# Kernel optimization log

Measured on AMD Instinct MI355X. Metric: run time of the kernel, lower is better.

The kernel has to match this reference:

```python
import jax, jax.numpy as jnp
import numpy as np

LN_EPS = 1e-5
GATE_EPS = 1e-9
TOP_K = 2
CAP_FACTOR = 1.0


def reference(x, gamma, beta, wg, W1, b1, W2, b2):
    B, S, H = x.shape
    E = wg.shape[1]
    T = B * S
    K = TOP_K
    C = int(np.ceil(K * T / E * CAP_FACTOR))  # per-expert capacity

    xf = x.reshape(T, H)
    # LayerNorm
    mu = jnp.mean(xf, axis=-1, keepdims=True)
    var = jnp.mean(jnp.square(xf - mu), axis=-1, keepdims=True)
    xn = (xf - mu) * jax.lax.rsqrt(var + LN_EPS) * gamma + beta

    # Gating (DeepSpeed top-k gate, softmax over experts)
    logits = xn @ wg                       # [T,E]
    gates = jax.nn.softmax(logits, axis=-1)
    vals, idx = jax.lax.top_k(gates, K)    # [T,K]

    # Capacity-aware positions: slot j priorities come after slots <j counts
    counts = jnp.zeros((E,), jnp.int32)
    pos_l, keep_l = [], []
    for j in range(K):
        oh = jax.nn.one_hot(idx[:, j], E, dtype=jnp.int32)  # [T,E]
        loc = jnp.cumsum(oh, axis=0) - 1 + counts[None, :]
        pos = jnp.sum(loc * oh, axis=1)                      # [T]
        counts = counts + jnp.sum(oh, axis=0)
        pos_l.append(pos)
        keep_l.append(pos < C)
    pos_k = jnp.stack(pos_l, axis=1)                         # [T,K]
    keep_k = jnp.stack(keep_l, axis=1)                       # [T,K]

    # Normalize kept gate values (DeepSpeed normalizes after capacity drop)
    kept = vals * keep_k.astype(vals.dtype)
    w = kept / (jnp.sum(kept, axis=1, keepdims=True) + GATE_EPS)  # [T,K]

    # Load-balancing aux loss (top-1 assignment counts, DeepSpeed style)
    me = jnp.mean(gates, axis=0)
    ce = jnp.mean(jax.nn.one_hot(idx[:, 0], E, dtype=gates.dtype), axis=0)
    l_aux = jnp.mean(me * ce) * E * E

    # Dispatch: scatter tokens into [E, C+1, H]; dropped tokens go to slot C (discarded)
    buf = jnp.zeros((E, C + 1, H), xn.dtype)
    pos_pad = jnp.where(keep_k, pos_k, C)                    # [T,K]
    for j in range(K):
        buf = buf.at[idx[:, j], pos_pad[:, j]].add(xn)

    # Grouped expert MLP
    h1 = jax.nn.gelu(jnp.einsum('ech,ehf->ecf', buf, W1) + b1[:, None, :], approximate=False)
    y = jnp.einsum('ecf,efh->ech', h1, W2) + b2[:, None, :]   # [E,C+1,H]

    # Combine: gather each token's expert outputs, weight, sum
    outf = jnp.zeros((T, H), x.dtype)
    for j in range(K):
        outf = outf + w[:, j, None] * y[idx[:, j], pos_pad[:, j]]

    out = x + outf.reshape(B, S, H)
    return out, l_aux, counts.astype(jnp.float32)


def setup_inputs() -> dict:
    key = jax.random.key(0)
    ks = jax.random.split(key, 6)
    H, E, F = 1024, 8, 4096
    x = jax.random.normal(ks[0], (2, 2048, H), jnp.float32)
    return {
        'x': x,
        'gamma': jnp.ones((H,), jnp.float32),
        'beta': jnp.zeros((H,), jnp.float32),
        'wg': jax.random.normal(ks[1], (H, E), jnp.float32) * 0.02,
        'W1': jax.random.normal(ks[2], (E, H, F), jnp.float32) * 0.02,
        'b1': jnp.zeros((E, F), jnp.float32),
        'W2': jax.random.normal(ks[3], (E, F, H), jnp.float32) * 0.02,
        'b2': jnp.zeros((E, H), jnp.float32),
    }
```

## Files before the change

### kernel.cpp

```cpp
#include <hip/hip_runtime.h>
#include <hip/hip_bf16.h>
#include <math.h>


#define T_TOK 4096
#define HD 1024
#define NE 8
#define FD 4096
#define CAPN 1024

typedef __attribute__((ext_vector_type(8))) short short8;
typedef __attribute__((ext_vector_type(4))) float f32x4;

__device__ __forceinline__ unsigned short f2b(float f) {
  __hip_bfloat16 h = __float2bfloat16(f);
  unsigned short u;
  __builtin_memcpy(&u, &h, 2);
  return u;
}

__global__ __launch_bounds__(256) void k_ln_gate(
    const float* __restrict__ x, const float* __restrict__ gamma,
    const float* __restrict__ beta, const float* __restrict__ wg,
    unsigned short* __restrict__ xn, float* __restrict__ gates,
    float2* __restrict__ vals, int2* __restrict__ eidx) {
  const int t = blockIdx.x;
  const int tid = threadIdx.x;
  const int lane = tid & 63, wid = tid >> 6;
  __shared__ float red[4];
  __shared__ float pr[4][8];

  const float4 v = ((const float4*)(x + (size_t)t * HD))[tid];
  float s = v.x + v.y + v.z + v.w;
#pragma unroll
  for (int o = 32; o > 0; o >>= 1) s += __shfl_down(s, o);
  if (lane == 0) red[wid] = s;
  __syncthreads();
  const float mean = (red[0] + red[1] + red[2] + red[3]) * (1.0f / HD);
  float dv[4];
  dv[0] = v.x - mean; dv[1] = v.y - mean; dv[2] = v.z - mean; dv[3] = v.w - mean;
  float q = dv[0]*dv[0] + dv[1]*dv[1] + dv[2]*dv[2] + dv[3]*dv[3];
  __syncthreads();
#pragma unroll
  for (int o = 32; o > 0; o >>= 1) q += __shfl_down(q, o);
  if (lane == 0) red[wid] = q;
  __syncthreads();
  const float var = (red[0] + red[1] + red[2] + red[3]) * (1.0f / HD);
  const float rs = 1.0f / sqrtf(var + 1e-5f);

  const float4 gm = ((const float4*)gamma)[tid];
  const float4 bt = ((const float4*)beta)[tid];
  float xv[4];
  xv[0] = dv[0] * rs * gm.x + bt.x;
  xv[1] = dv[1] * rs * gm.y + bt.y;
  xv[2] = dv[2] * rs * gm.z + bt.z;
  xv[3] = dv[3] * rs * gm.w + bt.w;
  ushort4 o4;
  o4.x = f2b(xv[0]); o4.y = f2b(xv[1]); o4.z = f2b(xv[2]); o4.w = f2b(xv[3]);
  ((ushort4*)(xn + (size_t)t * HD))[tid] = o4;

  float p[8];
#pragma unroll
  for (int e = 0; e < 8; e++) p[e] = 0.f;
  const int c0 = tid * 4;
#pragma unroll
  for (int i = 0; i < 4; i++) {
    const float4 w0 = ((const float4*)(wg + (size_t)(c0 + i) * NE))[0];
    const float4 w1 = ((const float4*)(wg + (size_t)(c0 + i) * NE))[1];
    p[0] += xv[i] * w0.x; p[1] += xv[i] * w0.y;
    p[2] += xv[i] * w0.z; p[3] += xv[i] * w0.w;
    p[4] += xv[i] * w1.x; p[5] += xv[i] * w1.y;
    p[6] += xv[i] * w1.z; p[7] += xv[i] * w1.w;
  }
#pragma unroll
  for (int e = 0; e < 8; e++)
#pragma unroll
    for (int o = 32; o > 0; o >>= 1) p[e] += __shfl_down(p[e], o);
  if (lane == 0) {
#pragma unroll
    for (int e = 0; e < 8; e++) pr[wid][e] = p[e];
  }
  __syncthreads();
  if (tid == 0) {
    float lg[8];
#pragma unroll
    for (int e = 0; e < 8; e++) lg[e] = pr[0][e] + pr[1][e] + pr[2][e] + pr[3][e];
    float mx = lg[0];
#pragma unroll
    for (int e = 1; e < 8; e++) mx = fmaxf(mx, lg[e]);
    float ex[8], sum = 0.f;
#pragma unroll
    for (int e = 0; e < 8; e++) { ex[e] = expf(lg[e] - mx); sum += ex[e]; }
    const float inv = 1.0f / sum;
    float g[8];
#pragma unroll
    for (int e = 0; e < 8; e++) { g[e] = ex[e] * inv; gates[(size_t)t * 8 + e] = g[e]; }
    int i0 = 0;
    for (int e = 1; e < 8; e++) if (g[e] > g[i0]) i0 = e;
    int i1 = (i0 == 0) ? 1 : 0;
    for (int e = 0; e < 8; e++) if (e != i0 && g[e] > g[i1]) i1 = e;
    vals[t] = make_float2(g[i0], g[i1]);
    eidx[t] = make_int2(i0, i1);
  }
}

__global__ __launch_bounds__(512) void k_scan(
    const int2* __restrict__ eidx, const float* __restrict__ gates,
    int* __restrict__ ppad, float* __restrict__ out_tail) {
  __shared__ short se0[T_TOK], se1[T_TOK];
  __shared__ int cc[2][64][8];
  __shared__ int cb[2][64][8];
  __shared__ float gsum[8][8];
  __shared__ int ctot[8], c0tot[8];
  const int tid = threadIdx.x, lane = tid & 63, wid = tid >> 6;
  for (int i = tid; i < T_TOK; i += 512) {
    int2 e2 = eidx[i];
    se0[i] = (short)e2.x; se1[i] = (short)e2.y;
  }
  __syncthreads();
  for (int c = wid * 8; c < wid * 8 + 8; ++c) {
    const int t = c * 64 + lane;
    const int e0 = se0[t], e1 = se1[t];
#pragma unroll
    for (int e = 0; e < 8; ++e) {
      unsigned long long m0 = __ballot(e0 == e);
      unsigned long long m1 = __ballot(e1 == e);
      if (lane == e) { cc[0][c][e] = __popcll(m0); cc[1][c][e] = __popcll(m1); }
    }
  }
  __syncthreads();
  {
    const int e = wid;
    int v0 = cc[0][lane][e], v1 = cc[1][lane][e];
    int p0 = v0, p1 = v1;
#pragma unroll
    for (int o = 1; o < 64; o <<= 1) {
      int u0 = __shfl_up(p0, o), u1 = __shfl_up(p1, o);
      if (lane >= o) { p0 += u0; p1 += u1; }
    }
    const int tot0 = __shfl(p0, 63), tot1 = __shfl(p1, 63);
    cb[0][lane][e] = p0 - v0;
    cb[1][lane][e] = p1 - v1 + tot0;
    if (lane == 0) { c0tot[e] = tot0; ctot[e] = tot0 + tot1; }
  }
  __syncthreads();
  for (int c = wid * 8; c < wid * 8 + 8; ++c) {
    const int t = c * 64 + lane;
    const unsigned long long lt = (lane == 63) ? 0x7fffffffffffffffull
                                               : ((1ull << lane) - 1ull);
    const int e0 = se0[t], e1 = se1[t];
    int p0 = 0, p1 = 0;
#pragma unroll
    for (int e = 0; e < 8; ++e) {
      unsigned long long m0 = __ballot(e0 == e);
      unsigned long long m1 = __ballot(e1 == e);
      if (e0 == e) p0 = cb[0][c][e] + __popcll(m0 & lt);
      if (e1 == e) p1 = cb[1][c][e] + __popcll(m1 & lt);
    }
    ppad[2 * t]     = (p0 < CAPN) ? p0 : CAPN;
    ppad[2 * t + 1] = (p1 < CAPN) ? p1 : CAPN;
  }
  float acc[8];
#pragma unroll
  for (int e = 0; e < 8; ++e) acc[e] = 0.f;
  for (int t = tid; t < T_TOK; t += 512) {
    const float4 a = ((const float4*)(gates + (size_t)t * 8))[0];
    const float4 b = ((const float4*)(gates + (size_t)t * 8))[1];
    acc[0] += a.x; acc[1] += a.y; acc[2] += a.z; acc[3] += a.w;
    acc[4] += b.x; acc[5] += b.y; acc[6] += b.z; acc[7] += b.w;
  }
#pragma unroll
  for (int e = 0; e < 8; ++e)
#pragma unroll
    for (int o = 32; o > 0; o >>= 1) acc[e] += __shfl_down(acc[e], o);
  if (lane == 0) {
#pragma unroll
    for (int e = 0; e < 8; ++e) gsum[wid][e] = acc[e];
  }
  __syncthreads();
  if (tid == 0) {
    float la = 0.f;
#pragma unroll
    for (int e = 0; e < 8; ++e) {
      float sg = 0.f;
#pragma unroll
      for (int w = 0; w < 8; ++w) sg += gsum[w][e];
      la += (sg * (1.0f / T_TOK)) * ((float)c0tot[e] * (1.0f / T_TOK));
    }
    out_tail[0] = la * 8.0f;
#pragma unroll
    for (int e = 0; e < 8; ++e) out_tail[1 + e] = (float)ctot[e];
  }
}

__global__ __launch_bounds__(128) void k_scatter(
    const unsigned short* __restrict__ xn, const int2* __restrict__ eidx,
    const int* __restrict__ ppad, unsigned short* __restrict__ buf) {
  const int b = blockIdx.x;
  const int t = b >> 1, j = b & 1;
  const int pp = ppad[2 * t + j];
  if (pp >= CAPN) return;
  const int2 e2 = eidx[t];
  const int e = j ? e2.y : e2.x;
  const uint4* s = (const uint4*)(xn + (size_t)t * HD);
  uint4* d = (uint4*)(buf + ((size_t)e * CAPN + pp) * HD);
  d[threadIdx.x] = s[threadIdx.x];
}

__global__ __launch_bounds__(256) void k_convT(
    const float* __restrict__ Win, unsigned short* __restrict__ Wout,
    int R, int C) {
  __shared__ __align__(16) unsigned short tile[64][72];
  const int e = blockIdx.z;
  const int c0 = blockIdx.x * 64, r0 = blockIdx.y * 64;
  const int tid = threadIdx.x;
  const int r = tid >> 2, qq = tid & 3;
  const float* src = Win + ((size_t)e * R + r0 + r) * C + c0;
#pragma unroll
  for (int i = 0; i < 4; i++) {
    const int cc = qq * 16 + i * 4;
    const float4 v = *(const float4*)(src + cc);
    tile[cc + 0][r] = f2b(v.x);
    tile[cc + 1][r] = f2b(v.y);
    tile[cc + 2][r] = f2b(v.z);
    tile[cc + 3][r] = f2b(v.w);
  }
  __syncthreads();
  const int cr = tid >> 3, q8 = tid & 7;
  unsigned short* dst0 = Wout + ((size_t)e * C + c0 + cr) * R + r0 + q8 * 8;
  *(uint4*)dst0 = *(const uint4*)&tile[cr][q8 * 8];
  unsigned short* dst1 = Wout + ((size_t)e * C + c0 + cr + 32) * R + r0 + q8 * 8;
  *(uint4*)dst1 = *(const uint4*)&tile[cr + 32][q8 * 8];
}

#define GLL(SRCP, DOFF) __builtin_amdgcn_global_load_lds( \
    (const __attribute__((address_space(1))) void*)(SRCP), \
    (__attribute__((address_space(3))) void*)(smem + (DOFF)), 16, 0, 0)

#define ST_A(S, KO) { \
  GLL(gA + (size_t)(KO) + stOff,             (S)*65536 + wid*1024); \
  GLL(gA + (size_t)(KO) + stOff + 64*LDK,    (S)*65536 + 8192 + wid*1024); \
  GLL(gA + (size_t)(KO) + stOff + 128*LDK,   (S)*65536 + 16384 + wid*1024); \
  GLL(gA + (size_t)(KO) + stOff + 192*LDK,   (S)*65536 + 24576 + wid*1024); }

#define ST_B(S, KO) { \
  GLL(gB + (size_t)(KO) + stOff,             (S)*65536 + 32768 + wid*1024); \
  GLL(gB + (size_t)(KO) + stOff + 64*LDK,    (S)*65536 + 40960 + wid*1024); \
  GLL(gB + (size_t)(KO) + stOff + 128*LDK,   (S)*65536 + 49152 + wid*1024); \
  GLL(gB + (size_t)(KO) + stOff + 192*LDK,   (S)*65536 + 57344 + wid*1024); }

#define RD_A(S, MH) { _Pragma("unroll") for (int f = 0; f < 4; ++f) { \
    aR[f*2+0] = *(const short8*)(smem + (S)*65536 + wrBase + ((MH)*4+f)*2048 + loff0); \
    aR[f*2+1] = *(const short8*)(smem + (S)*65536 + wrBase + ((MH)*4+f)*2048 + loff1); } }

#define RD_B(S, NH) { _Pragma("unroll") for (int g = 0; g < 2; ++g) { \
    bR[NH][g*2+0] = *(const short8*)(smem + (S)*65536 + 32768 + bBase + ((NH)*2+g)*2048 + loff0); \
    bR[NH][g*2+1] = *(const short8*)(smem + (S)*65536 + 32768 + bBase + ((NH)*2+g)*2048 + loff1); } }

#define MM(MH, NH) { __builtin_amdgcn_s_setprio(1); \
  _Pragma("unroll") for (int f = 0; f < 4; ++f) \
  _Pragma("unroll") for (int g = 0; g < 2; ++g) { \
    acc[(MH)*4+f][(NH)*2+g] = __builtin_amdgcn_mfma_f32_16x16x32_bf16(aR[f*2+0], bR[NH][g*2+0], acc[(MH)*4+f][(NH)*2+g], 0, 0, 0); \
    acc[(MH)*4+f][(NH)*2+g] = __builtin_amdgcn_mfma_f32_16x16x32_bf16(aR[f*2+1], bR[NH][g*2+1], acc[(MH)*4+f][(NH)*2+g], 0, 0, 0); } \
  __builtin_amdgcn_s_setprio(0); }

#define BARR __builtin_amdgcn_s_barrier()
#define LG0 asm volatile("s_waitcnt lgkmcnt(0)" ::: "memory")
#define VM8 asm volatile("s_waitcnt vmcnt(8)" ::: "memory")
#define VM0 asm volatile("s_waitcnt vmcnt(0)" ::: "memory")

#define ITER8(DOST, VM4TXT, VM8TXT, KK2, KK3) { \
  RD_A(0, 0); RD_B(0, 0); BARR; LG0; MM(0, 0); BARR; \
  RD_B(0, 1);             BARR; LG0; MM(0, 1); BARR; \
  RD_A(0, 1); if (DOST) { ST_B(0, KK2); } BARR; LG0; MM(1, 1); BARR; \
  if (DOST) { ST_A(0, KK2); } BARR; MM(1, 0); VM4TXT; BARR; \
  RD_A(1, 0); RD_B(1, 0); BARR; LG0; MM(0, 0); BARR; \
  RD_B(1, 1);             BARR; LG0; MM(0, 1); BARR; \
  RD_A(1, 1); if (DOST) { ST_B(1, KK3); } BARR; LG0; MM(1, 1); BARR; \
  if (DOST) { ST_A(1, KK3); } BARR; MM(1, 0); VM8TXT; BARR; }

template <int MODE, int SPLITK>
__global__ __launch_bounds__(512, 1) void k_gemm8p(
    const unsigned short* __restrict__ A, const unsigned short* __restrict__ Bt,
    const float* __restrict__ bias, void* __restrict__ out) {
  constexpr int LDK = MODE ? FD : HD;
  constexpr int N = MODE ? HD : FD;
  constexpr int KLOC = LDK / SPLITK;
  constexpr int NI = KLOC / 128;
  constexpr int NBT = N / 256;

  __shared__ __align__(16) unsigned char smem[131072];

  const int tid = threadIdx.x;
  const int lane = tid & 63, wid = tid >> 6;
  const int l15 = lane & 15, lq = (lane >> 4) & 3;
  const int wr = wid >> 2, wc = wid & 3;

  const int nwg = gridDim.x;
  const int per = nwg >> 3;
  const int lin = blockIdx.x;
  const int swz = (lin & 7) * per + (lin >> 3);
  const int mt = swz & 31;
  const int rest = swz >> 5;
  const int nt = rest % NBT;
  const int z = rest / NBT;

  const int e = mt >> 2;
  const size_t m0 = (size_t)mt * 256;
  const int n0 = nt * 256;
  const unsigned short* gA = A + m0 * (size_t)LDK + (size_t)z * KLOC;
  const unsigned short* gB = Bt + ((size_t)e * N + n0) * (size_t)LDK + (size_t)z * KLOC;

  const int stOff = (tid >> 3) * LDK + (((tid & 7) ^ ((tid >> 3) & 7)) << 3);

  const int loff0 = l15 * 128 + (((0 + lq) ^ (l15 & 7)) << 4);
  const int loff1 = l15 * 128 + (((4 + lq) ^ (l15 & 7)) << 4);
  const int wrBase = wr * 16384;
  const int bBase = (wc >> 1) * 16384 + (wc & 1) * 8192;

  short8 aR[8];
  short8 bR[2][8];
  f32x4 acc[8][4];
  const f32x4 fz = {0.f, 0.f, 0.f, 0.f};
#pragma unroll
  for (int mi = 0; mi < 8; mi++)
#pragma unroll
    for (int ni = 0; ni < 4; ni++) acc[mi][ni] = fz;

  ST_A(0, 0); ST_B(0, 0);
  ST_A(1, 64); ST_B(1, 64);
  VM8; BARR;

  int kk = 0;
  for (int it = 0; it < NI - 1; ++it, kk += 128) {
    ITER8(true, VM8, VM8, kk + 128, kk + 192);
  }
  ITER8(false, VM0, , 0, 0);

  const int colB = n0 + wc * 64 + l15;
  const size_t rowB = m0 + (size_t)wr * 128 + lq * 4;
  if (MODE == 0) {
    unsigned short* o = (unsigned short*)out;
    const float* brow = bias + (size_t)e * N;
#pragma unroll
    for (int mi = 0; mi < 8; ++mi)
#pragma unroll
      for (int ni = 0; ni < 4; ++ni) {
        const int col = colB + ni * 16;
        const float bv = brow[col];
#pragma unroll
        for (int r = 0; r < 4; ++r) {
          const size_t row = rowB + mi * 16 + r;
          const float pre = acc[mi][ni][r] + bv;
          const float g = 0.5f * pre * (1.0f + erff(pre * 0.70710678118654752f));
          o[row * (size_t)N + col] = f2b(g);
        }
      }
  } else {
    float* yp = (float*)out + (size_t)z * (8192ull * 1024ull);
#pragma unroll
    for (int mi = 0; mi < 8; ++mi)
#pragma unroll
      for (int ni = 0; ni < 4; ++ni) {
        const int col = colB + ni * 16;
#pragma unroll
        for (int r = 0; r < 4; ++r) {
          const size_t row = rowB + mi * 16 + r;
          yp[row * (size_t)N + col] = acc[mi][ni][r];
        }
      }
  }
}
#undef ITER8
#undef VM0
#undef VM8
#undef LG0
#undef BARR
#undef MM
#undef RD_B
#undef RD_A
#undef ST_B
#undef ST_A
#undef GLL

template <int SPLIT>
__global__ __launch_bounds__(256) void k_combine(
    const float* __restrict__ x, const float* __restrict__ y0,
    const float* __restrict__ y1, const float* __restrict__ b2,
    const int2* __restrict__ eidx, const int* __restrict__ ppad,
    const float2* __restrict__ vals, float* __restrict__ out) {
  const int t = blockIdx.x, tid = threadIdx.x;
  const float2 v = vals[t];
  const int2 e2 = eidx[t];
  const int p0 = ppad[2 * t], p1 = ppad[2 * t + 1];
  const float k0 = (p0 < CAPN) ? v.x : 0.f;
  const float k1 = (p1 < CAPN) ? v.y : 0.f;
  const float inv = 1.0f / (k0 + k1 + 1e-9f);
  const float w0 = k0 * inv, w1 = k1 * inv;
  float4 o = ((const float4*)(x + (size_t)t * HD))[tid];
  if (p0 < CAPN) {
    const size_t s = ((size_t)e2.x * CAPN + p0) * HD;
    float4 a = ((const float4*)(y0 + s))[tid];
    if (SPLIT == 2) {
      const float4 b = ((const float4*)(y1 + s))[tid];
      a.x += b.x; a.y += b.y; a.z += b.z; a.w += b.w;
    }
    const float4 bb = ((const float4*)(b2 + (size_t)e2.x * HD))[tid];
    o.x += w0 * (a.x + bb.x); o.y += w0 * (a.y + bb.y);
    o.z += w0 * (a.z + bb.z); o.w += w0 * (a.w + bb.w);
  }
  if (p1 < CAPN) {
    const size_t s = ((size_t)e2.y * CAPN + p1) * HD;
    float4 a = ((const float4*)(y0 + s))[tid];
    if (SPLIT == 2) {
      const float4 b = ((const float4*)(y1 + s))[tid];
      a.x += b.x; a.y += b.y; a.z += b.z; a.w += b.w;
    }
    const float4 bb = ((const float4*)(b2 + (size_t)e2.y * HD))[tid];
    o.x += w1 * (a.x + bb.x); o.y += w1 * (a.y + bb.y);
    o.z += w1 * (a.z + bb.z); o.w += w1 * (a.w + bb.w);
  }
  ((float4*)(out + (size_t)t * HD))[tid] = o;
}

extern "C" void kernel_launch(void* const* d_in, const int* in_sizes, int n_in,
                              void* d_out, int out_size, void* d_ws, size_t ws_size,
                              hipStream_t stream) {
  const float* x     = (const float*)d_in[0];
  const float* gamma = (const float*)d_in[1];
  const float* beta  = (const float*)d_in[2];
  const float* wg    = (const float*)d_in[3];
  const float* W1    = (const float*)d_in[4];
  const float* b1    = (const float*)d_in[5];
  const float* W2    = (const float*)d_in[6];
  const float* b2    = (const float*)d_in[7];
  float* out = (float*)d_out;

  char* ws = (char*)d_ws;
  float* gates        = (float*)(ws);
  float2* vals        = (float2*)(ws + (128ull << 10));
  int2* eidx          = (int2*)(ws + (160ull << 10));
  int* ppad           = (int*)(ws + (192ull << 10));
  unsigned short* xn  = (unsigned short*)(ws + (512ull << 10));
  unsigned short* buf = (unsigned short*)(ws + (512ull << 10) + (8ull << 20));
  unsigned short* h1  = (unsigned short*)(ws + (512ull << 10) + (24ull << 20));
  unsigned short* WT  = (unsigned short*)(ws + (512ull << 10) + (88ull << 20));
  float* y0           = (float*)(ws + (512ull << 10) + (152ull << 20));
  float* y1           = (float*)(ws + (512ull << 10) + (184ull << 20));
  const bool splitk = ws_size >= ((217ull << 20));

  k_ln_gate<<<T_TOK, 256, 0, stream>>>(x, gamma, beta, wg, xn, gates, vals, eidx);
  k_scan<<<1, 512, 0, stream>>>(eidx, gates, ppad, out + (size_t)T_TOK * HD);
  k_scatter<<<T_TOK * 2, 128, 0, stream>>>(xn, eidx, ppad, buf);
  k_convT<<<dim3(FD / 64, HD / 64, NE), 256, 0, stream>>>(W1, WT, HD, FD);
  k_gemm8p<0, 1><<<512, 512, 0, stream>>>(buf, WT, b1, h1);
  k_convT<<<dim3(HD / 64, FD / 64, NE), 256, 0, stream>>>(W2, WT, FD, HD);
  if (splitk) {
    k_gemm8p<1, 2><<<256, 512, 0, stream>>>(h1, WT, nullptr, y0);
    k_combine<2><<<T_TOK, 256, 0, stream>>>(x, y0, y1, b2, eidx, ppad, vals, out);
  } else {
    k_gemm8p<1, 1><<<128, 512, 0, stream>>>(h1, WT, nullptr, y0);
    k_combine<1><<<T_TOK, 256, 0, stream>>>(x, y0, y1, b2, eidx, ppad, vals, out);
  }
}
```

Measured before the change: 530.9 us.

## Stage GEMM epilogue through LDS, store split-K partials as bf16, restructure gate reduction

```diff
diff --git a/kernel.cpp b/kernel.cpp
--- a/kernel.cpp
+++ b/kernel.cpp
@@ -17,6 +17,12 @@
   unsigned short u;
   __builtin_memcpy(&u, &h, 2);
   return u;
+}
+__device__ __forceinline__ float b2f(unsigned short u) {
+  unsigned v = ((unsigned)u) << 16;
+  float f;
+  __builtin_memcpy(&f, &v, 4);
+  return f;
 }
 
 __global__ __launch_bounds__(256) void k_ln_gate(
@@ -28,7 +34,7 @@
   const int tid = threadIdx.x;
   const int lane = tid & 63, wid = tid >> 6;
   __shared__ float red[4];
-  __shared__ float pr[4][8];
+  __shared__ float pr2[256][9];
 
   const float4 v = ((const float4*)(x + (size_t)t * HD))[tid];
   float s = v.x + v.y + v.z + v.w;
@@ -73,34 +79,37 @@
     p[6] += xv[i] * w1.z; p[7] += xv[i] * w1.w;
   }
 #pragma unroll
-  for (int e = 0; e < 8; e++)
-#pragma unroll
-    for (int o = 32; o > 0; o >>= 1) p[e] += __shfl_down(p[e], o);
-  if (lane == 0) {
-#pragma unroll
-    for (int e = 0; e < 8; e++) pr[wid][e] = p[e];
-  }
-  __syncthreads();
-  if (tid == 0) {
-    float lg[8];
-#pragma unroll
-    for (int e = 0; e < 8; e++) lg[e] = pr[0][e] + pr[1][e] + pr[2][e] + pr[3][e];
-    float mx = lg[0];
-#pragma unroll
-    for (int e = 1; e < 8; e++) mx = fmaxf(mx, lg[e]);
-    float ex[8], sum = 0.f;
-#pragma unroll
-    for (int e = 0; e < 8; e++) { ex[e] = expf(lg[e] - mx); sum += ex[e]; }
-    const float inv = 1.0f / sum;
-    float g[8];
-#pragma unroll
-    for (int e = 0; e < 8; e++) { g[e] = ex[e] * inv; gates[(size_t)t * 8 + e] = g[e]; }
-    int i0 = 0;
-    for (int e = 1; e < 8; e++) if (g[e] > g[i0]) i0 = e;
-    int i1 = (i0 == 0) ? 1 : 0;
-    for (int e = 0; e < 8; e++) if (e != i0 && g[e] > g[i1]) i1 = e;
-    vals[t] = make_float2(g[i0], g[i1]);
-    eidx[t] = make_int2(i0, i1);
+  for (int e = 0; e < 8; e++) pr2[tid][e] = p[e];
+  __syncthreads();
+  if (wid == 0) {
+    const int e8 = lane & 7, g8 = lane >> 3;
+    float s2 = 0.f;
+#pragma unroll
+    for (int i = 0; i < 32; ++i) s2 += pr2[g8 + 8 * i][e8];
+    s2 += __shfl_xor(s2, 8);
+    s2 += __shfl_xor(s2, 16);
+    s2 += __shfl_xor(s2, 32);
+    float lgv[8];
+#pragma unroll
+    for (int e = 0; e < 8; e++) lgv[e] = __shfl(s2, e);
+    if (lane == 0) {
+      float mx = lgv[0];
+#pragma unroll
+      for (int e = 1; e < 8; e++) mx = fmaxf(mx, lgv[e]);
+      float ex[8], sum = 0.f;
+#pragma unroll
+      for (int e = 0; e < 8; e++) { ex[e] = expf(lgv[e] - mx); sum += ex[e]; }
+      const float inv = 1.0f / sum;
+      float g[8];
+#pragma unroll
+      for (int e = 0; e < 8; e++) { g[e] = ex[e] * inv; gates[(size_t)t * 8 + e] = g[e]; }
+      int i0 = 0;
+      for (int e = 1; e < 8; e++) if (g[e] > g[i0]) i0 = e;
+      int i1 = (i0 == 0) ? 1 : 0;
+      for (int e = 0; e < 8; e++) if (e != i0 && g[e] > g[i1]) i1 = e;
+      vals[t] = make_float2(g[i0], g[i1]);
+      eidx[t] = make_int2(i0, i1);
+    }
   }
 }
 
@@ -196,15 +205,12 @@
 __global__ __launch_bounds__(128) void k_scatter(
     const unsigned short* __restrict__ xn, const int2* __restrict__ eidx,
     const int* __restrict__ ppad, unsigned short* __restrict__ buf) {
-  const int b = blockIdx.x;
-  const int t = b >> 1, j = b & 1;
-  const int pp = ppad[2 * t + j];
-  if (pp >= CAPN) return;
+  const int t = blockIdx.x;
   const int2 e2 = eidx[t];
-  const int e = j ? e2.y : e2.x;
-  const uint4* s = (const uint4*)(xn + (size_t)t * HD);
-  uint4* d = (uint4*)(buf + ((size_t)e * CAPN + pp) * HD);
-  d[threadIdx.x] = s[threadIdx.x];
+  const int p0 = ppad[2 * t], p1 = ppad[2 * t + 1];
+  const uint4 v = ((const uint4*)(xn + (size_t)t * HD))[threadIdx.x];
+  if (p0 < CAPN) ((uint4*)(buf + ((size_t)e2.x * CAPN + p0) * HD))[threadIdx.x] = v;
+  if (p1 < CAPN) ((uint4*)(buf + ((size_t)e2.y * CAPN + p1) * HD))[threadIdx.x] = v;
 }
 
 __global__ __launch_bounds__(256) void k_convT(
@@ -282,7 +288,7 @@
 template <int MODE, int SPLITK>
 __global__ __launch_bounds__(512, 1) void k_gemm8p(
     const unsigned short* __restrict__ A, const unsigned short* __restrict__ Bt,
-    const float* __restrict__ bias, void* __restrict__ out) {
+    const float* __restrict__ bias, unsigned short* __restrict__ out) {
   constexpr int LDK = MODE ? FD : HD;
   constexpr int N = MODE ? HD : FD;
   constexpr int KLOC = LDK / SPLITK;
@@ -296,12 +302,11 @@
   const int l15 = lane & 15, lq = (lane >> 4) & 3;
   const int wr = wid >> 2, wc = wid & 3;
 
-  const int nwg = gridDim.x;
-  const int per = nwg >> 3;
   const int lin = blockIdx.x;
-  const int swz = (lin & 7) * per + (lin >> 3);
-  const int mt = swz & 31;
-  const int rest = swz >> 5;
+  const int xcd = lin & 7;
+  const int i = lin >> 3;
+  const int mt = (xcd << 2) | (i & 3);
+  const int rest = i >> 2;
   const int nt = rest % NBT;
   const int z = rest / NBT;
 
@@ -312,7 +317,6 @@
   const unsigned short* gB = Bt + ((size_t)e * N + n0) * (size_t)LDK + (size_t)z * KLOC;
 
   const int stOff = (tid >> 3) * LDK + (((tid & 7) ^ ((tid >> 3) & 7)) << 3);
-
   const int loff0 = l15 * 128 + (((0 + lq) ^ (l15 & 7)) << 4);
   const int loff1 = l15 * 128 + (((4 + lq) ^ (l15 & 7)) << 4);
   const int wrBase = wr * 16384;
@@ -337,38 +341,44 @@
   }
   ITER8(false, VM0, , 0, 0);
 
-  const int colB = n0 + wc * 64 + l15;
-  const size_t rowB = m0 + (size_t)wr * 128 + lq * 4;
+  unsigned short* o = out + (MODE ? (size_t)z * (8192ull * 1024ull) : 0);
+  float bv[4];
   if (MODE == 0) {
-    unsigned short* o = (unsigned short*)out;
     const float* brow = bias + (size_t)e * N;
 #pragma unroll
-    for (int mi = 0; mi < 8; ++mi)
+    for (int ni = 0; ni < 4; ++ni) bv[ni] = brow[n0 + wc * 64 + ni * 16 + l15];
+  }
+  unsigned char* wbuf = smem + wid * 8192;
+#pragma unroll
+  for (int pass = 0; pass < 2; ++pass) {
+#pragma unroll
+    for (int mi4 = 0; mi4 < 4; ++mi4) {
 #pragma unroll
       for (int ni = 0; ni < 4; ++ni) {
-        const int col = colB + ni * 16;
-        const float bv = brow[col];
+        const int cslot = ((ni ^ lq) << 4) + l15;
 #pragma unroll
         for (int r = 0; r < 4; ++r) {
-          const size_t row = rowB + mi * 16 + r;
-          const float pre = acc[mi][ni][r] + bv;
-          const float g = 0.5f * pre * (1.0f + erff(pre * 0.70710678118654752f));
-          o[row * (size_t)N + col] = f2b(g);
+          const int lr = mi4 * 16 + lq * 4 + r;
+          float vv = acc[pass * 4 + mi4][ni][r];
+          if (MODE == 0) {
+            vv += bv[ni];
+            vv = 0.5f * vv * (1.0f + erff(vv * 0.70710678118654752f));
+          }
+          *(unsigned short*)(wbuf + lr * 128 + cslot * 2) = f2b(vv);
         }
       }
-  } else {
-    float* yp = (float*)out + (size_t)z * (8192ull * 1024ull);
-#pragma unroll
-    for (int mi = 0; mi < 8; ++mi)
-#pragma unroll
-      for (int ni = 0; ni < 4; ++ni) {
-        const int col = colB + ni * 16;
-#pragma unroll
-        for (int r = 0; r < 4; ++r) {
-          const size_t row = rowB + mi * 16 + r;
-          yp[row * (size_t)N + col] = acc[mi][ni][r];
-        }
-      }
+    }
+    asm volatile("s_waitcnt lgkmcnt(0)" ::: "memory");
+#pragma unroll
+    for (int ii = 0; ii < 8; ++ii) {
+      const int lr = ii * 8 + (lane >> 3);
+      const uint4 d = *(const uint4*)(wbuf + lr * 128 + (lane & 7) * 16);
+      const int lqr = (lr >> 2) & 3;
+      const int colo = ((((lane >> 1) & 3) ^ lqr) << 4) + (lane & 1) * 8;
+      const size_t row = m0 + (size_t)wr * 128 + pass * 64 + lr;
+      *(uint4*)(o + row * (size_t)N + n0 + wc * 64 + colo) = d;
+    }
+    asm volatile("s_waitcnt lgkmcnt(0)" ::: "memory");
   }
 }
 #undef ITER8
@@ -385,8 +395,8 @@
 
 template <int SPLIT>
 __global__ __launch_bounds__(256) void k_combine(
-    const float* __restrict__ x, const float* __restrict__ y0,
-    const float* __restrict__ y1, const float* __restrict__ b2,
+    const float* __restrict__ x, const unsigned short* __restrict__ y0,
+    const unsigned short* __restrict__ y1, const float* __restrict__ b2,
     const int2* __restrict__ eidx, const int* __restrict__ ppad,
     const float2* __restrict__ vals, float* __restrict__ out) {
   const int t = blockIdx.x, tid = threadIdx.x;
@@ -400,25 +410,27 @@
   float4 o = ((const float4*)(x + (size_t)t * HD))[tid];
   if (p0 < CAPN) {
     const size_t s = ((size_t)e2.x * CAPN + p0) * HD;
-    float4 a = ((const float4*)(y0 + s))[tid];
+    const ushort4 a = ((const ushort4*)(y0 + s))[tid];
+    float ax = b2f(a.x), ay = b2f(a.y), az = b2f(a.z), aw = b2f(a.w);
     if (SPLIT == 2) {
-      const float4 b = ((const float4*)(y1 + s))[tid];
-      a.x += b.x; a.y += b.y; a.z += b.z; a.w += b.w;
+      const ushort4 b = ((const ushort4*)(y1 + s))[tid];
+      ax += b2f(b.x); ay += b2f(b.y); az += b2f(b.z); aw += b2f(b.w);
     }
     const float4 bb = ((const float4*)(b2 + (size_t)e2.x * HD))[tid];
-    o.x += w0 * (a.x + bb.x); o.y += w0 * (a.y + bb.y);
-    o.z += w0 * (a.z + bb.z); o.w += w0 * (a.w + bb.w);
+    o.x += w0 * (ax + bb.x); o.y += w0 * (ay + bb.y);
+    o.z += w0 * (az + bb.z); o.w += w0 * (aw + bb.w);
   }
   if (p1 < CAPN) {
     const size_t s = ((size_t)e2.y * CAPN + p1) * HD;
-    float4 a = ((const float4*)(y0 + s))[tid];
+    const ushort4 a = ((const ushort4*)(y0 + s))[tid];
+    float ax = b2f(a.x), ay = b2f(a.y), az = b2f(a.z), aw = b2f(a.w);
     if (SPLIT == 2) {
-      const float4 b = ((const float4*)(y1 + s))[tid];
-      a.x += b.x; a.y += b.y; a.z += b.z; a.w += b.w;
+      const ushort4 b = ((const ushort4*)(y1 + s))[tid];
+      ax += b2f(b.x); ay += b2f(b.y); az += b2f(b.z); aw += b2f(b.w);
     }
     const float4 bb = ((const float4*)(b2 + (size_t)e2.y * HD))[tid];
-    o.x += w1 * (a.x + bb.x); o.y += w1 * (a.y + bb.y);
-    o.z += w1 * (a.z + bb.z); o.w += w1 * (a.w + bb.w);
+    o.x += w1 * (ax + bb.x); o.y += w1 * (ay + bb.y);
+    o.z += w1 * (az + bb.z); o.w += w1 * (aw + bb.w);
   }
   ((float4*)(out + (size_t)t * HD))[tid] = o;
 }
@@ -445,13 +457,13 @@
   unsigned short* buf = (unsigned short*)(ws + (512ull << 10) + (8ull << 20));
   unsigned short* h1  = (unsigned short*)(ws + (512ull << 10) + (24ull << 20));
   unsigned short* WT  = (unsigned short*)(ws + (512ull << 10) + (88ull << 20));
-  float* y0           = (float*)(ws + (512ull << 10) + (152ull << 20));
-  float* y1           = (float*)(ws + (512ull << 10) + (184ull << 20));
-  const bool splitk = ws_size >= ((217ull << 20));
+  unsigned short* y0  = (unsigned short*)(ws + (512ull << 10) + (152ull << 20));
+  unsigned short* y1  = (unsigned short*)(ws + (512ull << 10) + (168ull << 20));
+  const bool splitk = ws_size >= (186ull << 20);
 
   k_ln_gate<<<T_TOK, 256, 0, stream>>>(x, gamma, beta, wg, xn, gates, vals, eidx);
   k_scan<<<1, 512, 0, stream>>>(eidx, gates, ppad, out + (size_t)T_TOK * HD);
-  k_scatter<<<T_TOK * 2, 128, 0, stream>>>(xn, eidx, ppad, buf);
+  k_scatter<<<T_TOK, 128, 0, stream>>>(xn, eidx, ppad, buf);
   k_convT<<<dim3(FD / 64, HD / 64, NE), 256, 0, stream>>>(W1, WT, HD, FD);
   k_gemm8p<0, 1><<<512, 512, 0, stream>>>(buf, WT, b1, h1);
   k_convT<<<dim3(HD / 64, FD / 64, NE), 256, 0, stream>>>(W2, WT, FD, HD);
```

Measured after the change: 517.3 us. 1.03x faster.
